# Optimization experiments

Hardware: AMD Instinct MI355X
Metric: run time of the kernel (lower is better)

## Reference

```python
import jax, jax.numpy as jnp
import numpy as np
import math

DIM = 512
BLOCK_NUM = 16
SEQ_LEN = 8192
BLOCK_LEN = SEQ_LEN // BLOCK_NUM  # 512 == DIM -> mask used as-is
BATCH = 4
LN_EPS = 1e-3  # keras LayerNormalization default epsilon


def setup_inputs() -> dict:
    key = jax.random.key(0)
    ks = jax.random.split(key, 5)
    inputs = jax.random.normal(ks[0], (BATCH, BLOCK_NUM, BLOCK_LEN, DIM), dtype=jnp.float32)
    # binary padding-style mask, values in {0,1}
    mask_array = jax.random.randint(ks[1], (BATCH, SEQ_LEN, DIM), 0, 2).astype(jnp.float32)
    scale = 1.0 / math.sqrt(DIM)
    dw1 = jax.random.normal(ks[2], (DIM, DIM), dtype=jnp.float32) * scale
    dw2 = jax.random.normal(ks[3], (DIM, DIM), dtype=jnp.float32) * scale
    dw3 = jax.random.normal(ks[4], (DIM, DIM), dtype=jnp.float32) * scale
    db1 = jnp.zeros((DIM,), dtype=jnp.float32)
    db2 = jnp.zeros((DIM,), dtype=jnp.float32)
    db3 = jnp.zeros((DIM,), dtype=jnp.float32)
    return {"inputs": inputs, "mask_array": mask_array,
            "dw1": dw1, "dw2": dw2, "dw3": dw3,
            "db1": db1, "db2": db2, "db3": db3}


def reference(inputs, mask_array, dw1, dw2, dw3, db1, db2, db3):
    # inputs: [B, block_num, block_len, dim]
    Q = jnp.matmul(inputs, dw1) + db1
    K = jnp.matmul(inputs, dw2) + db2
    V = jnpp_matmul = jnp.matmul(inputs, dw3) + db3
    V = jnp.matmul(inputs, dw3) + db3
    # block-local attention scores: [B, bn, bl, bl]
    scores = jnp.einsum('bnqd,bnkd->bnqk', Q, K) / math.sqrt(DIM)
    # mask: [B, seq_len, dim] -> [B, bn, bl, dim]; block_len == dim so no slice/tile
    m = mask_array.reshape(BATCH, BLOCK_NUM, BLOCK_LEN, DIM)
    scores = scores + (1.0 - m) * jnp.float32(-1e10)
    p = jax.nn.softmax(scores, axis=-1)
    out = jnp.einsum('bnqk,bnkd->bnqd', p, V) + inputs  # residual
    # LayerNorm(axis=-1), fresh keras layer: gamma=1, beta=0, eps=1e-3
    mean = jnp.mean(out, axis=-1, keepdims=True)
    var = jnp.mean(jnp.square(out - mean), axis=-1, keepdims=True)
    return (out - mean) / jnp.sqrt(var + LN_EPS)
```

## Files before the change

kernel.cpp:

```cpp
#include <hip/hip_runtime.h>

#define DIMK 512
#define NBLK 64
#define NTOK 32768

typedef short  short8 __attribute__((ext_vector_type(8)));
typedef float  f32x4  __attribute__((ext_vector_type(4)));
typedef unsigned short u16x8 __attribute__((ext_vector_type(8)));

__device__ __forceinline__ unsigned short f2bf(float f) {
  union { float f; unsigned u; } v; v.f = f;
  unsigned r = (v.u + 0x7FFFu + ((v.u >> 16) & 1u)) >> 16;
  return (unsigned short)r;
}
__device__ __forceinline__ float bf2f(unsigned short h) {
  return __uint_as_float(((unsigned)h) << 16);
}

__device__ __forceinline__ void gload_lds16(const unsigned short* g,
                                            unsigned short* l) {
  __builtin_amdgcn_global_load_lds(
      (const __attribute__((address_space(1))) unsigned int*)(g),
      (__attribute__((address_space(3))) unsigned int*)(l),
      16, 0, 0);
}

__global__ __launch_bounds__(256) void k_wt_prep(
    const float* __restrict__ dw1, const float* __restrict__ dw2,
    const float* __restrict__ dw3, unsigned short* __restrict__ Wt)
{
  const int idx = blockIdx.x * 256 + threadIdx.x;
  const int w = idx >> 18;
  const int r = idx & 262143;
  const int n = r >> 9, k = r & 511;
  const float* dw = (w == 0) ? dw1 : (w == 1) ? dw2 : dw3;
  Wt[(size_t)w * 262144 + (size_t)n * 512 + k] = f2bf(dw[(size_t)k * 512 + n]);
}

__global__ __launch_bounds__(256) void k_xconv(
    const float* __restrict__ X, unsigned short* __restrict__ Xb)
{
  const size_t i = ((size_t)blockIdx.x * 256 + threadIdx.x) * 8;
  const float4 a = *(const float4*)(X + i);
  const float4 b = *(const float4*)(X + i + 4);
  u16x8 o;
  o[0] = f2bf(a.x); o[1] = f2bf(a.y); o[2] = f2bf(a.z); o[3] = f2bf(a.w);
  o[4] = f2bf(b.x); o[5] = f2bf(b.y); o[6] = f2bf(b.z); o[7] = f2bf(b.w);
  *(u16x8*)(Xb + i) = o;
}

__global__ __launch_bounds__(256) void k_bitpack(
    const float* __restrict__ mask, unsigned char* __restrict__ bits)
{
  const size_t gid = (size_t)blockIdx.x * 256 + threadIdx.x;
  const size_t i = gid * 8;
  const float4 ma = *(const float4*)(mask + i);
  const float4 mb = *(const float4*)(mask + i + 4);
  unsigned v = 0;
  v |= (ma.x > 0.5f) << 0; v |= (ma.y > 0.5f) << 1;
  v |= (ma.z > 0.5f) << 2; v |= (ma.w > 0.5f) << 3;
  v |= (mb.x > 0.5f) << 4; v |= (mb.y > 0.5f) << 5;
  v |= (mb.z > 0.5f) << 6; v |= (mb.w > 0.5f) << 7;
  bits[gid] = (unsigned char)v;
}

__global__ __launch_bounds__(256, 2) void k_qkv(
    const unsigned short* __restrict__ Xb, const unsigned short* __restrict__ Wt,
    const float* __restrict__ db1, const float* __restrict__ db2,
    const float* __restrict__ db3,
    unsigned short* __restrict__ Qb, unsigned short* __restrict__ Kb,
    unsigned short* __restrict__ Vt)
{
  __shared__ __align__(16) unsigned short smem[128 * 136];
  unsigned short* As = smem;
  unsigned short* Bs = smem + 4096;

  const int id = blockIdx.x;
  const int x = id & 7, j = id >> 3;
  const int mtile = x * 32 + (j >> 2);
  const int nt = j & 3;
  const size_t m0 = (size_t)mtile * 128;
  const int n0 = nt * 128;

  const int tid = threadIdx.x, lane = tid & 63, wv = tid >> 6;
  const int quad = lane >> 4, l16 = lane & 15;
  const int rb = (wv >> 1) * 64, cb = (wv & 1) * 64;

  f32x4 acc[3][4][4];
#pragma unroll
  for (int w = 0; w < 3; ++w)
#pragma unroll
    for (int i = 0; i < 4; ++i)
#pragma unroll
      for (int jj = 0; jj < 4; ++jj) {
        f32x4 z = {0.f, 0.f, 0.f, 0.f}; acc[w][i][jj] = z;
      }

  const int ra0 = tid >> 2,          oa0 = (tid & 3) << 3;
  const int ra1 = (tid + 256) >> 2,  oa1 = ((tid + 256) & 3) << 3;
  const unsigned short* a0 = &Xb[(m0 + ra0) * (size_t)DIMK + oa0];
  const unsigned short* a1 = &Xb[(m0 + ra1) * (size_t)DIMK + oa1];

  for (int it = 0; it < 16; ++it) {
    const int k0 = it * 32;
    gload_lds16(a0 + k0, &As[tid * 8]);
    gload_lds16(a1 + k0, &As[(tid + 256) * 8]);
#pragma unroll
    for (int h = 0; h < 6; ++h) {
      const int c = tid + h * 256;
      const int w = c >> 9, cc = c & 511;
      const int r = cc >> 2, o = (cc & 3) << 3;
      gload_lds16(&Wt[(size_t)w * 262144 + (size_t)(n0 + r) * 512 + k0 + o],
                  &Bs[w * 4096 + cc * 8]);
    }
    __syncthreads();
    short8 af[4];
#pragma unroll
    for (int i = 0; i < 4; ++i)
      af[i] = *(const short8*)&As[(rb + i * 16 + l16) * 32 + quad * 8];
#pragma unroll
    for (int jj = 0; jj < 4; ++jj)
#pragma unroll
      for (int w = 0; w < 3; ++w) {
        const short8 bf =
            *(const short8*)&Bs[w * 4096 + (cb + jj * 16 + l16) * 32 + quad * 8];
#pragma unroll
        for (int i = 0; i < 4; ++i)
          acc[w][i][jj] = __builtin_amdgcn_mfma_f32_16x16x32_bf16(
              af[i], bf, acc[w][i][jj], 0, 0, 0);
      }
    __syncthreads();
  }

#pragma unroll
  for (int w = 0; w < 2; ++w) {
    const float* db = (w == 0) ? db1 : db2;
    unsigned short* Ob = (w == 0) ? Qb : Kb;
#pragma unroll
    for (int i = 0; i < 4; ++i)
#pragma unroll
      for (int jj = 0; jj < 4; ++jj)
#pragma unroll
        for (int r = 0; r < 4; ++r) {
          const size_t row = m0 + rb + i * 16 + quad * 4 + r;
          const int col = n0 + cb + jj * 16 + l16;
          Ob[row * (size_t)DIMK + col] = f2bf(acc[w][i][jj][r] + db[col]);
        }
  }
#pragma unroll
  for (int i = 0; i < 4; ++i)
#pragma unroll
    for (int jj = 0; jj < 4; ++jj) {
      const int cl = cb + jj * 16 + l16;
      const int t0 = rb + i * 16 + quad * 4;
      const float bv = db3[n0 + cl];
      ushort4 pk;
      pk.x = f2bf(acc[2][i][jj][0] + bv);
      pk.y = f2bf(acc[2][i][jj][1] + bv);
      pk.z = f2bf(acc[2][i][jj][2] + bv);
      pk.w = f2bf(acc[2][i][jj][3] + bv);
      *(ushort4*)&smem[cl * 136 + t0] = pk;
    }
  __syncthreads();
  const int blk = mtile >> 2;
  const int tokbase = (mtile & 3) * 128;
  unsigned short* Vblk = Vt + (size_t)blk * 262144;
#pragma unroll
  for (int h = 0; h < 8; ++h) {
    const int c = tid + h * 256;
    const int cl = c >> 4, toff = (c & 15) * 8;
    *(u16x8*)&Vblk[(size_t)(n0 + cl) * 512 + tokbase + toff] =
        *(const u16x8*)&smem[cl * 136 + toff];
  }
}

__global__ __launch_bounds__(256, 2) void k_attn_p(
    const unsigned short* __restrict__ Qb, const unsigned short* __restrict__ Kb,
    const unsigned long long* __restrict__ bits, unsigned short* __restrict__ Pb)
{
  __shared__ __align__(16) unsigned short As[64 * 32];
  __shared__ __align__(16) unsigned short Bs[512 * 32];
  __shared__ float red[4][64];
  const int tid = threadIdx.x, lane = tid & 63, wv = tid >> 6;
  const int quad = lane >> 4, l16 = lane & 15;
  const int blk = blockIdx.x & 63, mt = blockIdx.x >> 6;
  const size_t tb = (size_t)blk * 512;
  const size_t q0 = tb + (size_t)mt * 64;

  f32x4 acc[4][8];
#pragma unroll
  for (int i = 0; i < 4; ++i)
#pragma unroll
    for (int j = 0; j < 8; ++j) { f32x4 z = {0.f, 0.f, 0.f, 0.f}; acc[i][j] = z; }

  const int ra = tid >> 2, oa = (tid & 3) << 3;
  const unsigned short* ap = &Qb[(q0 + ra) * (size_t)DIMK + oa];
  const unsigned short* kp = &Kb[tb * (size_t)DIMK];

  for (int it = 0; it < 16; ++it) {
    const int k0 = it * 32;
    gload_lds16(ap + k0, &As[tid * 8]);
#pragma unroll
    for (int h = 0; h < 8; ++h) {
      const int c = tid + h * 256;
      const int r = c >> 2, o = (c & 3) << 3;
      gload_lds16(kp + (size_t)r * DIMK + k0 + o, &Bs[c * 8]);
    }
    __syncthreads();
    short8 af[4], bfv[8];
#pragma unroll
    for (int i = 0; i < 4; ++i)
      af[i] = *(const short8*)&As[(i * 16 + l16) * 32 + quad * 8];
#pragma unroll
    for (int j = 0; j < 8; ++j)
      bfv[j] = *(const short8*)&Bs[(wv * 128 + j * 16 + l16) * 32 + quad * 8];
#pragma unroll
    for (int i = 0; i < 4; ++i)
#pragma unroll
      for (int j = 0; j < 8; ++j)
        acc[i][j] = __builtin_amdgcn_mfma_f32_16x16x32_bf16(
            af[i], bfv[j], acc[i][j], 0, 0, 0);
    __syncthreads();
  }

  const float scale = 0.04419417382415922f;
  float rmax[4][4];
#pragma unroll
  for (int i = 0; i < 4; ++i)
#pragma unroll
    for (int r = 0; r < 4; ++r) rmax[i][r] = -3.0e38f;
#pragma unroll
  for (int i = 0; i < 4; ++i)
#pragma unroll
    for (int r = 0; r < 4; ++r) {
      const size_t tok = q0 + i * 16 + quad * 4 + r;
      const unsigned long long w0 = bits[tok * 8 + wv * 2];
      const unsigned long long w1 = bits[tok * 8 + wv * 2 + 1];
#pragma unroll
      for (int j = 0; j < 8; ++j) {
        const unsigned long long sel = (j < 4) ? w0 : w1;
        const float bias = ((sel >> (l16 + 16 * (j & 3))) & 1ull) ? 0.0f : -1e10f;
        const float v = acc[i][j][r] * scale + bias;
        acc[i][j][r] = v;
        rmax[i][r] = fmaxf(rmax[i][r], v);
      }
    }
#pragma unroll
  for (int i = 0; i < 4; ++i)
#pragma unroll
    for (int r = 0; r < 4; ++r)
      for (int d = 1; d < 16; d <<= 1)
        rmax[i][r] = fmaxf(rmax[i][r], __shfl_xor(rmax[i][r], d, 64));
  if (l16 == 0)
#pragma unroll
    for (int i = 0; i < 4; ++i)
#pragma unroll
      for (int r = 0; r < 4; ++r) red[wv][i * 16 + quad * 4 + r] = rmax[i][r];
  __syncthreads();
#pragma unroll
  for (int i = 0; i < 4; ++i)
#pragma unroll
    for (int r = 0; r < 4; ++r) {
      const int row = i * 16 + quad * 4 + r;
      rmax[i][r] = fmaxf(fmaxf(red[0][row], red[1][row]),
                         fmaxf(red[2][row], red[3][row]));
    }
  __syncthreads();
  float rsum[4][4];
#pragma unroll
  for (int i = 0; i < 4; ++i)
#pragma unroll
    for (int r = 0; r < 4; ++r) rsum[i][r] = 0.f;
#pragma unroll
  for (int i = 0; i < 4; ++i)
#pragma unroll
    for (int j = 0; j < 8; ++j)
#pragma unroll
      for (int r = 0; r < 4; ++r) {
        const float e = __expf(acc[i][j][r] - rmax[i][r]);
        acc[i][j][r] = e;
        rsum[i][r] += e;
      }
#pragma unroll
  for (int i = 0; i < 4; ++i)
#pragma unroll
    for (int r = 0; r < 4; ++r)
      for (int d = 1; d < 16; d <<= 1)
        rsum[i][r] += __shfl_xor(rsum[i][r], d, 64);
  if (l16 == 0)
#pragma unroll
    for (int i = 0; i < 4; ++i)
#pragma unroll
      for (int r = 0; r < 4; ++r) red[wv][i * 16 + quad * 4 + r] = rsum[i][r];
  __syncthreads();
#pragma unroll
  for (int i = 0; i < 4; ++i)
#pragma unroll
    for (int r = 0; r < 4; ++r) {
      const int row = i * 16 + quad * 4 + r;
      rsum[i][r] = 1.0f / (red[0][row] + red[1][row] + red[2][row] + red[3][row]);
    }
#pragma unroll
  for (int i = 0; i < 4; ++i)
#pragma unroll
    for (int j = 0; j < 8; ++j)
#pragma unroll
      for (int r = 0; r < 4; ++r) {
        const size_t tok = q0 + i * 16 + quad * 4 + r;
        const int col = wv * 128 + j * 16 + l16;
        Pb[tok * (size_t)DIMK + col] = f2bf(acc[i][j][r] * rsum[i][r]);
      }
}

__global__ __launch_bounds__(256, 2) void k_pv_ln(
    const unsigned short* __restrict__ Pb, const unsigned short* __restrict__ Vt,
    const unsigned short* __restrict__ Xb, float* __restrict__ Out)
{
  __shared__ __align__(16) unsigned short As[64 * 32];
  __shared__ __align__(16) unsigned short Bs[512 * 32];
  __shared__ float2 red[4][64];
  const int tid = threadIdx.x, lane = tid & 63, wv = tid >> 6;
  const int quad = lane >> 4, l16 = lane & 15;
  const int blk = blockIdx.x & 63, mt = blockIdx.x >> 6;
  const size_t tb = (size_t)blk * 512;
  const size_t q0 = tb + (size_t)mt * 64;

  f32x4 acc[4][8];
#pragma unroll
  for (int i = 0; i < 4; ++i)
#pragma unroll
    for (int j = 0; j < 8; ++j) { f32x4 z = {0.f, 0.f, 0.f, 0.f}; acc[i][j] = z; }

  const int ra = tid >> 2, oa = (tid & 3) << 3;
  const unsigned short* ap = &Pb[(q0 + ra) * (size_t)DIMK + oa];
  const unsigned short* vp = Vt + (size_t)blk * 262144;

  for (int it = 0; it < 16; ++it) {
    const int k0 = it * 32;
    gload_lds16(ap + k0, &As[tid * 8]);
#pragma unroll
    for (int h = 0; h < 8; ++h) {
      const int c = tid + h * 256;
      const int r = c >> 2, o = (c & 3) << 3;
      gload_lds16(vp + (size_t)r * DIMK + k0 + o, &Bs[c * 8]);
    }
    __syncthreads();
    short8 af[4], bfv[8];
#pragma unroll
    for (int i = 0; i < 4; ++i)
      af[i] = *(const short8*)&As[(i * 16 + l16) * 32 + quad * 8];
#pragma unroll
    for (int j = 0; j < 8; ++j)
      bfv[j] = *(const short8*)&Bs[(wv * 128 + j * 16 + l16) * 32 + quad * 8];
#pragma unroll
    for (int i = 0; i < 4; ++i)
#pragma unroll
      for (int j = 0; j < 8; ++j)
        acc[i][j] = __builtin_amdgcn_mfma_f32_16x16x32_bf16(
            af[i], bfv[j], acc[i][j], 0, 0, 0);
    __syncthreads();
  }

  float vsum[4][4], vsq[4][4];
#pragma unroll
  for (int i = 0; i < 4; ++i)
#pragma unroll
    for (int r = 0; r < 4; ++r) { vsum[i][r] = 0.f; vsq[i][r] = 0.f; }
#pragma unroll
  for (int i = 0; i < 4; ++i)
#pragma unroll
    for (int j = 0; j < 8; ++j)
#pragma unroll
      for (int r = 0; r < 4; ++r) {
        const size_t tok = q0 + i * 16 + quad * 4 + r;
        const int col = wv * 128 + j * 16 + l16;
        const float v = acc[i][j][r] + bf2f(Xb[tok * (size_t)DIMK + col]);
        acc[i][j][r] = v;
        vsum[i][r] += v;
        vsq[i][r] += v * v;
      }
#pragma unroll
  for (int i = 0; i < 4; ++i)
#pragma unroll
    for (int r = 0; r < 4; ++r)
      for (int d = 1; d < 16; d <<= 1) {
        vsum[i][r] += __shfl_xor(vsum[i][r], d, 64);
        vsq[i][r]  += __shfl_xor(vsq[i][r], d, 64);
      }
  if (l16 == 0)
#pragma unroll
    for (int i = 0; i < 4; ++i)
#pragma unroll
      for (int r = 0; r < 4; ++r) {
        float2 p; p.x = vsum[i][r]; p.y = vsq[i][r];
        red[wv][i * 16 + quad * 4 + r] = p;
      }
  __syncthreads();
#pragma unroll
  for (int i = 0; i < 4; ++i)
#pragma unroll
    for (int r = 0; r < 4; ++r) {
      const int row = i * 16 + quad * 4 + r;
      float s = 0.f, q = 0.f;
#pragma unroll
      for (int w = 0; w < 4; ++w) { s += red[w][row].x; q += red[w][row].y; }
      const float mean = s * (1.0f / 512.0f);
      const float var  = q * (1.0f / 512.0f) - mean * mean;
      vsum[i][r] = mean;
      vsq[i][r]  = rsqrtf(var + 1e-3f);
    }
#pragma unroll
  for (int i = 0; i < 4; ++i)
#pragma unroll
    for (int j = 0; j < 8; ++j)
#pragma unroll
      for (int r = 0; r < 4; ++r) {
        const size_t tok = q0 + i * 16 + quad * 4 + r;
        const int col = wv * 128 + j * 16 + l16;
        Out[tok * (size_t)DIMK + col] =
            (acc[i][j][r] - vsum[i][r]) * vsq[i][r];
      }
}

extern "C" void kernel_launch(void* const* d_in, const int* in_sizes, int n_in,
                              void* d_out, int out_size, void* d_ws, size_t ws_size,
                              hipStream_t stream)
{
  const float* X    = (const float*)d_in[0];
  const float* mask = (const float*)d_in[1];
  const float* dw1  = (const float*)d_in[2];
  const float* dw2  = (const float*)d_in[3];
  const float* dw3  = (const float*)d_in[4];
  const float* db1  = (const float*)d_in[5];
  const float* db2  = (const float*)d_in[6];
  const float* db3  = (const float*)d_in[7];
  float* Out = (float*)d_out;

  char* ws = (char*)d_ws;
  const size_t MB = 1ull << 20;
  unsigned short* Wt = (unsigned short*)(ws);
  unsigned short* Qb = (unsigned short*)(ws + 2 * MB);
  unsigned short* Kb = (unsigned short*)(ws + 34 * MB);
  unsigned short* Vt = (unsigned short*)(ws + 66 * MB);
  unsigned short* Xb = (unsigned short*)(ws + 98 * MB);
  unsigned short* Pb = Qb;
  unsigned char*  bits = (unsigned char*)d_out;

  k_wt_prep<<<3072, 256, 0, stream>>>(dw1, dw2, dw3, Wt);
  k_xconv  <<<8192, 256, 0, stream>>>(X, Xb);
  k_bitpack<<<8192, 256, 0, stream>>>(mask, bits);
  k_qkv    <<<1024, 256, 0, stream>>>(Xb, Wt, db1, db2, db3, Qb, Kb, Vt);
  k_attn_p <<<512, 256, 0, stream>>>(Qb, Kb, (const unsigned long long*)bits, Pb);
  k_pv_ln  <<<512, 256, 0, stream>>>(Pb, Vt, Xb, Out);
}
```

Baseline: 344.8 us.

## Double-buffer LDS tiles in GEMM kernels and tile weight transpose through shared memory

Adds double-buffered shared-memory staging to the QKV, QK^T and PV GEMM loops, so global-to-LDS loads for the next K slice are issued before the MFMAs on the current slice, replacing one of the two barriers' serialization of load and compute. Separately rewrites the weight transpose/convert kernel to use a padded 64x64 shared tile for coalesced reads and writes. Double buffering doubles LDS use per block (64KB for k_qkv, ~74KB for the attention kernels), which may reduce occupancy below the launch_bounds target of 2 blocks per CU.

```diff
diff --git a/kernel.cpp b/kernel.cpp
--- a/kernel.cpp
+++ b/kernel.cpp
@@ -29,12 +29,33 @@
     const float* __restrict__ dw1, const float* __restrict__ dw2,
     const float* __restrict__ dw3, unsigned short* __restrict__ Wt)
 {
-  const int idx = blockIdx.x * 256 + threadIdx.x;
-  const int w = idx >> 18;
-  const int r = idx & 262143;
-  const int n = r >> 9, k = r & 511;
+  __shared__ float t[64][65];
+  const int b = blockIdx.x;
+  const int w = b >> 6;
+  const int tt = b & 63;
+  const int kt = (tt >> 3) * 64;
+  const int nt = (tt & 7) * 64;
   const float* dw = (w == 0) ? dw1 : (w == 1) ? dw2 : dw3;
-  Wt[(size_t)w * 262144 + (size_t)n * 512 + k] = f2bf(dw[(size_t)k * 512 + n]);
+  const int tid = threadIdx.x;
+  const int rr = tid >> 4;
+  const int cc = (tid & 15) << 2;
+
+#pragma unroll
+  for (int p = 0; p < 4; ++p) {
+    const int r = rr + p * 16;
+    const float4 v = *(const float4*)&dw[(size_t)(kt + r) * 512 + nt + cc];
+    t[cc + 0][r] = v.x; t[cc + 1][r] = v.y;
+    t[cc + 2][r] = v.z; t[cc + 3][r] = v.w;
+  }
+  __syncthreads();
+#pragma unroll
+  for (int p = 0; p < 4; ++p) {
+    const int r = rr + p * 16;
+    ushort4 o;
+    o.x = f2bf(t[r][cc + 0]); o.y = f2bf(t[r][cc + 1]);
+    o.z = f2bf(t[r][cc + 2]); o.w = f2bf(t[r][cc + 3]);
+    *(ushort4*)&Wt[(size_t)w * 262144 + (size_t)(nt + r) * 512 + kt + cc] = o;
+  }
 }
 
 __global__ __launch_bounds__(256) void k_xconv(
@@ -71,9 +92,7 @@
     unsigned short* __restrict__ Qb, unsigned short* __restrict__ Kb,
     unsigned short* __restrict__ Vt)
 {
-  __shared__ __align__(16) unsigned short smem[128 * 136];
-  unsigned short* As = smem;
-  unsigned short* Bs = smem + 4096;
+  __shared__ __align__(16) unsigned short smem[32768];
 
   const int id = blockIdx.x;
   const int x = id & 7, j = id >> 3;
@@ -101,19 +120,28 @@
   const unsigned short* a0 = &Xb[(m0 + ra0) * (size_t)DIMK + oa0];
   const unsigned short* a1 = &Xb[(m0 + ra1) * (size_t)DIMK + oa1];
 
-  for (int it = 0; it < 16; ++it) {
+  auto stage = [&](unsigned short* base, int it) {
     const int k0 = it * 32;
-    gload_lds16(a0 + k0, &As[tid * 8]);
-    gload_lds16(a1 + k0, &As[(tid + 256) * 8]);
+    gload_lds16(a0 + k0, base + tid * 8);
+    gload_lds16(a1 + k0, base + (tid + 256) * 8);
 #pragma unroll
     for (int h = 0; h < 6; ++h) {
       const int c = tid + h * 256;
       const int w = c >> 9, cc = c & 511;
       const int r = cc >> 2, o = (cc & 3) << 3;
       gload_lds16(&Wt[(size_t)w * 262144 + (size_t)(n0 + r) * 512 + k0 + o],
-                  &Bs[w * 4096 + cc * 8]);
-    }
-    __syncthreads();
+                  base + 4096 + w * 4096 + cc * 8);
+    }
+  };
+
+  stage(smem, 0);
+  __syncthreads();
+  int cur = 0;
+  for (int it = 0; it < 16; ++it) {
+    unsigned short* cbuf = smem + cur * 16384;
+    if (it < 15) stage(smem + (cur ^ 1) * 16384, it + 1);
+    const unsigned short* As = cbuf;
+    const unsigned short* Bs = cbuf + 4096;
     short8 af[4];
 #pragma unroll
     for (int i = 0; i < 4; ++i)
@@ -130,6 +158,7 @@
               af[i], bf, acc[w][i][jj], 0, 0, 0);
       }
     __syncthreads();
+    cur ^= 1;
   }
 
 #pragma unroll
@@ -178,8 +207,7 @@
     const unsigned short* __restrict__ Qb, const unsigned short* __restrict__ Kb,
     const unsigned long long* __restrict__ bits, unsigned short* __restrict__ Pb)
 {
-  __shared__ __align__(16) unsigned short As[64 * 32];
-  __shared__ __align__(16) unsigned short Bs[512 * 32];
+  __shared__ __align__(16) unsigned short smem[36864];
   __shared__ float red[4][64];
   const int tid = threadIdx.x, lane = tid & 63, wv = tid >> 6;
   const int quad = lane >> 4, l16 = lane & 15;
@@ -197,16 +225,25 @@
   const unsigned short* ap = &Qb[(q0 + ra) * (size_t)DIMK + oa];
   const unsigned short* kp = &Kb[tb * (size_t)DIMK];
 
-  for (int it = 0; it < 16; ++it) {
+  auto stage = [&](unsigned short* base, int it) {
     const int k0 = it * 32;
-    gload_lds16(ap + k0, &As[tid * 8]);
+    gload_lds16(ap + k0, base + tid * 8);
 #pragma unroll
     for (int h = 0; h < 8; ++h) {
       const int c = tid + h * 256;
       const int r = c >> 2, o = (c & 3) << 3;
-      gload_lds16(kp + (size_t)r * DIMK + k0 + o, &Bs[c * 8]);
-    }
-    __syncthreads();
+      gload_lds16(kp + (size_t)r * DIMK + k0 + o, base + 2048 + c * 8);
+    }
+  };
+
+  stage(smem, 0);
+  __syncthreads();
+  int cur = 0;
+  for (int it = 0; it < 16; ++it) {
+    unsigned short* cbuf = smem + cur * 18432;
+    if (it < 15) stage(smem + (cur ^ 1) * 18432, it + 1);
+    const unsigned short* As = cbuf;
+    const unsigned short* Bs = cbuf + 2048;
     short8 af[4], bfv[8];
 #pragma unroll
     for (int i = 0; i < 4; ++i)
@@ -221,6 +258,7 @@
         acc[i][j] = __builtin_amdgcn_mfma_f32_16x16x32_bf16(
             af[i], bfv[j], acc[i][j], 0, 0, 0);
     __syncthreads();
+    cur ^= 1;
   }
 
   const float scale = 0.04419417382415922f;
@@ -316,8 +354,7 @@
     const unsigned short* __restrict__ Pb, const unsigned short* __restrict__ Vt,
     const unsigned short* __restrict__ Xb, float* __restrict__ Out)
 {
-  __shared__ __align__(16) unsigned short As[64 * 32];
-  __shared__ __align__(16) unsigned short Bs[512 * 32];
+  __shared__ __align__(16) unsigned short smem[36864];
   __shared__ float2 red[4][64];
   const int tid = threadIdx.x, lane = tid & 63, wv = tid >> 6;
   const int quad = lane >> 4, l16 = lane & 15;
@@ -335,16 +372,25 @@
   const unsigned short* ap = &Pb[(q0 + ra) * (size_t)DIMK + oa];
   const unsigned short* vp = Vt + (size_t)blk * 262144;
 
-  for (int it = 0; it < 16; ++it) {
+  auto stage = [&](unsigned short* base, int it) {
     const int k0 = it * 32;
-    gload_lds16(ap + k0, &As[tid * 8]);
+    gload_lds16(ap + k0, base + tid * 8);
 #pragma unroll
     for (int h = 0; h < 8; ++h) {
       const int c = tid + h * 256;
       const int r = c >> 2, o = (c & 3) << 3;
-      gload_lds16(vp + (size_t)r * DIMK + k0 + o, &Bs[c * 8]);
-    }
-    __syncthreads();
+      gload_lds16(vp + (size_t)r * DIMK + k0 + o, base + 2048 + c * 8);
+    }
+  };
+
+  stage(smem, 0);
+  __syncthreads();
+  int cur = 0;
+  for (int it = 0; it < 16; ++it) {
+    unsigned short* cbuf = smem + cur * 18432;
+    if (it < 15) stage(smem + (cur ^ 1) * 18432, it + 1);
+    const unsigned short* As = cbuf;
+    const unsigned short* Bs = cbuf + 2048;
     short8 af[4], bfv[8];
 #pragma unroll
     for (int i = 0; i < 4; ++i)
@@ -359,6 +405,7 @@
         acc[i][j] = __builtin_amdgcn_mfma_f32_16x16x32_bf16(
             af[i], bfv[j], acc[i][j], 0, 0, 0);
     __syncthreads();
+    cur ^= 1;
   }
 
   float vsum[4][4], vsq[4][4];
@@ -446,7 +493,7 @@
   unsigned short* Pb = Qb;
   unsigned char*  bits = (unsigned char*)d_out;
 
-  k_wt_prep<<<3072, 256, 0, stream>>>(dw1, dw2, dw3, Wt);
+  k_wt_prep<<<192, 256, 0, stream>>>(dw1, dw2, dw3, Wt);
   k_xconv  <<<8192, 256, 0, stream>>>(X, Xb);
   k_bitpack<<<8192, 256, 0, stream>>>(mask, bits);
   k_qkv    <<<1024, 256, 0, stream>>>(Xb, Wt, db1, db2, db3, Qb, Kb, Vt);
```

Result: faster. 326.6 us (-5.3%).
